# Performance work log

Measured on AMD Instinct MI355X. Metric: run time of the kernel, lower is better.

## Reference

```python
import jax, jax.numpy as jnp
import numpy as np

N, D_IN, D, E, B = 30000, 512, 512, 300000, 4096
N_RES, N_DNN = 2, 2
EPS = 1e-5


def _ln(x, g, b):
    mu = jnp.mean(x, axis=-1, keepdims=True)
    var = jnp.mean((x - mu) ** 2, axis=-1, keepdims=True)
    return (x - mu) * jax.lax.rsqrt(var + EPS) * g + b


def setup_inputs() -> dict:
    key = jax.random.key(0)
    ks = jax.random.split(key, 16)
    s = 1.0 / np.sqrt(D)
    inp = {
        "node_feat": jax.random.normal(ks[0], (N, D_IN), jnp.float32),
        "edge_hop0": jax.random.randint(ks[1], (2, E), 0, N, jnp.int32),
        "edge_hop1": jax.random.randint(ks[2], (2, E), 0, N, jnp.int32),
        "target_idx": jax.random.randint(ks[3], (B,), 0, N, jnp.int32),
        # node transform
        "Wt": jax.random.normal(ks[4], (D_IN, D), jnp.float32) / np.sqrt(D_IN),
        "bt": jnp.zeros((D,), jnp.float32),
        # GATConv (shared across both hops, one relation)
        "Wf": jax.random.normal(ks[5], (D, D), jnp.float32) * s,
        "bf": jnp.zeros((D,), jnp.float32),
        "w_att": jax.random.normal(ks[6], (2 * D,), jnp.float32) * s,
        "b_att": jnp.zeros((), jnp.float32),
        "gat_bias": jnp.zeros((D,), jnp.float32),
        # Res_DNN
        "Wp": jax.random.normal(ks[7], (D, D), jnp.float32) * s,
        "bp": jnp.zeros((D,), jnp.float32),
        "dnn_W": jax.random.normal(ks[8], (N_RES, N_DNN, D, D), jnp.float32) * s,
        "dnn_b": jnp.zeros((N_RES, N_DNN, D), jnp.float32),
        "dnn_g": jnp.ones((N_RES, N_DNN, D), jnp.float32),
        "dnn_beta": jnp.zeros((N_RES, N_DNN, D), jnp.float32),
        "res_g": jnp.ones((N_RES, D), jnp.float32),
        "res_beta": jnp.zeros((N_RES, D), jnp.float32),
        "Wc": jax.random.normal(ks[9], (D, 1), jnp.float32) * s,
        "bc": jnp.zeros((1,), jnp.float32),
    }
    return inp


def _gat(feat, edges, Wf, bf, w_att, b_att, gat_bias):
    # dst and src are the same node set / same features here
    h = feat @ Wf + bf                      # [N, D]
    di, si = edges[0], edges[1]             # [E], [E]
    # att(concat(dst_h, src_h)) == dst_h @ w[:D] + src_h @ w[D:] + b
    sd = h @ w_att[:D]                      # [N]
    ss = h @ w_att[D:]                      # [N]
    e = jnp.tanh(sd[di] + ss[si] + b_att)   # [E]
    # sparse softmax per destination row
    m = jax.ops.segment_max(e, di, num_segments=N)
    a = jnp.exp(e - m[di])
    denom = jax.ops.segment_sum(a, di, num_segments=N)
    alpha = a / denom[di]                   # [E]
    # sparse-mm aggregation
    out = jax.ops.segment_sum(alpha[:, None] * h[si], di, num_segments=N)
    return out + gat_bias


def reference(node_feat, edge_hop0, edge_hop1, target_idx, Wt, bt, Wf, bf,
              w_att, b_att, gat_bias, Wp, bp, dnn_W, dnn_b, dnn_g, dnn_beta,
              res_g, res_beta, Wc, bc):
    # node-type feature transform (dropout is identity at inference)
    feat = node_feat @ Wt + bt              # [N, D]
    # hops processed from last to first: hop1 then hop0
    for edges in (edge_hop1, edge_hop0):
        g = _gat(feat, edges, Wf, bf, w_att, b_att, gat_bias)
        feat = (feat + g) * 0.5             # mean of stacked [orig, gat_out]
    h = feat[target_idx]                    # [B, D]
    # Res_DNN head
    h = h @ Wp + bp
    for r in range(N_RES):
        sc = h
        for i in range(N_DNN):
            h = _ln(jnp.tanh(h @ dnn_W[r, i] + dnn_b[r, i]), dnn_g[r, i], dnn_beta[r, i])
        h = _ln(jnp.tanh(sc + h), res_g[r], res_beta[r])
    logits = h @ Wc + bc                    # [B, 1]
    return jax.nn.sigmoid(logits)
```

## Files before the change

### kernel.cpp

```cpp
#include <hip/hip_runtime.h>

#define D 512
typedef unsigned short ushort_t;
typedef __attribute__((ext_vector_type(8))) short bf16x8;
typedef __attribute__((ext_vector_type(4))) float f32x4;

static __device__ __forceinline__ ushort_t f2bf(float f) {
  unsigned u = __float_as_uint(f);
  u += 0x7fffu + ((u >> 16) & 1u);
  return (ushort_t)(u >> 16);
}
static __device__ __forceinline__ float bf2f(ushort_t h) {
  return __uint_as_float(((unsigned)h) << 16);
}

static __device__ __forceinline__ void gld_lds16(const void* g, void* lds) {
  __builtin_amdgcn_global_load_lds(
      (const __attribute__((address_space(1))) unsigned int*)g,
      (__attribute__((address_space(3))) unsigned int*)lds, 16, 0, 0);
}

__global__ __launch_bounds__(256) void pack_weight7(
    const float* __restrict__ Wt, const float* __restrict__ Wf,
    const float* __restrict__ Wp, const float* __restrict__ Wd,
    ushort_t* __restrict__ out) {
  const int per = D * D;
  int i = blockIdx.x * 256 + threadIdx.x;
  if (i >= per * 7) return;
  const int mat = i / per;
  const int r = i - mat * per;
  const float* W;
  if (mat == 0) W = Wt;
  else if (mat == 1) W = Wf;
  else if (mat == 2) W = Wp;
  else W = Wd + (size_t)(mat - 3) * per;
  const int k = r / D, n = r - k * D;
  const int nt = n >> 4, col = n & 15, kt = k >> 5, kg = (k >> 3) & 3, j = k & 7;
  out[(size_t)mat * per + (((size_t)nt * (D >> 5) + kt) << 9) + ((kg << 4) + col) * 8 + j] =
      f2bf(W[r]);
}

__global__ __launch_bounds__(256) void conv_bf16_pad(
    const float* __restrict__ in, ushort_t* __restrict__ out, int M, int Mp, int K) {
  const size_t i4 = ((size_t)blockIdx.x * 256 + threadIdx.x) * 4;
  if (i4 >= (size_t)Mp * K) return;
  const int row = (int)(i4 / K);
  ushort4 o;
  if (row < M) {
    const float4 v = *reinterpret_cast<const float4*>(&in[i4]);
    o.x = f2bf(v.x); o.y = f2bf(v.y); o.z = f2bf(v.z); o.w = f2bf(v.w);
  } else {
    o.x = o.y = o.z = o.w = 0;
  }
  *reinterpret_cast<ushort4*>(&out[i4]) = o;
}

__global__ __launch_bounds__(256) void init_buffers(
    int* __restrict__ cnt, int* __restrict__ tflag, int* __restrict__ nflag,
    int* __restrict__ counters, int Nn, int N2) {
  const int i = blockIdx.x * 256 + threadIdx.x;
  if (i < N2) cnt[i] = 0;
  if (i < Nn) { tflag[i] = 0; nflag[i] = 0; }
  if (i < 2) counters[i * 64] = 0;
}

__global__ void fill_bucket(const int* __restrict__ e1, const int* __restrict__ e0,
                            const int* __restrict__ tidx, int* __restrict__ tflag,
                            int* __restrict__ cnt, int* __restrict__ bucket,
                            int Nn, int E, int B) {
  const int e = blockIdx.x * blockDim.x + threadIdx.x;
  if (e < B) tflag[tidx[e]] = 1;
  if (e >= E) return;
  const int d1 = e1[e];
  const int p1 = atomicAdd(&cnt[d1], 1);
  if (p1 < 64) bucket[(size_t)d1 * 64 + p1] = e1[E + e];
  const int d0 = e0[e];
  const int p0 = atomicAdd(&cnt[Nn + d0], 1);
  if (p0 < 64) bucket[((size_t)(Nn + d0)) * 64 + p0] = e0[E + e];
}

__global__ void flag_srcs(const int* __restrict__ e0, const int* __restrict__ tflag,
                          int* __restrict__ nflag, int E) {
  const int e = blockIdx.x * blockDim.x + threadIdx.x;
  if (e < E && tflag[e0[e]]) nflag[e0[E + e]] = 1;
}

__global__ void compact2(const int* __restrict__ tflag, const int* __restrict__ nflag,
                         int* __restrict__ tlist, int* __restrict__ nlist,
                         int* __restrict__ counters, int Nn) {
  const int i = blockIdx.x * 256 + threadIdx.x;
  if (i >= Nn) return;
  const int tf = tflag[i];
  if (tf) tlist[atomicAdd(&counters[0], 1)] = i;
  if (tf | nflag[i]) nlist[atomicAdd(&counters[64], 1)] = i;
}

__global__ __launch_bounds__(512) void gemm_mfma(
    const ushort_t* __restrict__ A, const ushort_t* __restrict__ Bp,
    const float* __restrict__ bias, ushort_t* __restrict__ C16,
    const float* __restrict__ watt, float* __restrict__ sd_part,
    float* __restrict__ ss_part, int Mp, int N, int K) {
  __shared__ __align__(16) ushort_t As[2][8 * 512];
  __shared__ __align__(16) ushort_t Bs[2][8 * 512];
  const int nwg = gridDim.x;
  const int q = nwg >> 3, rm = nwg & 7;
  const int xcd = blockIdx.x & 7, kk = blockIdx.x >> 3;
  const int lin = (xcd < rm ? xcd * (q + 1) : rm * (q + 1) + (xcd - rm) * q) + kk;
  const int m0 = (lin >> 2) * 128;
  const int n0 = (lin & 3) * 128;
  const int tid = threadIdx.x;
  const int lane = tid & 63;
  const int wid = tid >> 6;
  const int wm = wid >> 1;
  const int wn = wid & 1;
  const int arow = lane & 15;
  const int akoff = (lane >> 4) * 8;
  const int c15 = lane & 15;
  const int rgrp = lane >> 4;
  const int kt32 = K >> 5;
  f32x4 acc[2][4] = {};

  auto stage = [&](int kt, int b) {
    const int k0 = kt * 32;
    gld_lds16(&A[(size_t)(m0 + wid * 16 + arow) * K + k0 + akoff],
              &As[b][wid * 512]);
    gld_lds16(&Bp[(((size_t)(n0 / 16 + wid) * kt32 + kt) << 9) + lane * 8],
              &Bs[b][wid * 512]);
  };

  stage(0, 0);
  __syncthreads();
  int cur = 0;
  for (int t = 0; t < kt32; ++t) {
    if (t + 1 < kt32) stage(t + 1, cur ^ 1);
    bf16x8 af[2], bfr[4];
#pragma unroll
    for (int mi = 0; mi < 2; ++mi)
      af[mi] = *reinterpret_cast<const bf16x8*>(&As[cur][(wm * 2 + mi) * 512 + lane * 8]);
#pragma unroll
    for (int ni = 0; ni < 4; ++ni)
      bfr[ni] = *reinterpret_cast<const bf16x8*>(&Bs[cur][(wn * 4 + ni) * 512 + lane * 8]);
#pragma unroll
    for (int mi = 0; mi < 2; ++mi)
#pragma unroll
      for (int ni = 0; ni < 4; ++ni)
        acc[mi][ni] = __builtin_amdgcn_mfma_f32_16x16x32_bf16(af[mi], bfr[ni], acc[mi][ni], 0, 0, 0);
    __syncthreads();
    cur ^= 1;
  }
  const int band = (n0 >> 6) + wn;
#pragma unroll
  for (int mi = 0; mi < 2; ++mi) {
    const int row = m0 + wm * 32 + mi * 16 + (rgrp << 2);
#pragma unroll
    for (int r = 0; r < 4; ++r) {
      float psd = 0.f, pss = 0.f;
#pragma unroll
      for (int ni = 0; ni < 4; ++ni) {
        const int col = n0 + wn * 64 + ni * 16 + c15;
        const float v = acc[mi][ni][r] + bias[col];
        C16[(size_t)(row + r) * N + col] = f2bf(v);
        if (watt) {
          psd += v * watt[col];
          pss += v * watt[D + col];
        }
      }
      if (watt) {
#pragma unroll
        for (int off = 8; off > 0; off >>= 1) {
          psd += __shfl_xor(psd, off);
          pss += __shfl_xor(pss, off);
        }
        if (c15 == 0) {
          sd_part[(size_t)band * Mp + row + r] = psd;
          ss_part[(size_t)band * Mp + row + r] = pss;
        }
      }
    }
  }
}

__global__ __launch_bounds__(256) void combine_dots(
    const float* __restrict__ sd_part, const float* __restrict__ ss_part,
    float* __restrict__ sd, float* __restrict__ ss, int Mp, int Nn) {
  const int i = blockIdx.x * 256 + threadIdx.x;
  if (i >= Nn) return;
  float a = 0.f, b = 0.f;
#pragma unroll
  for (int bnd = 0; bnd < 8; ++bnd) {
    a += sd_part[(size_t)bnd * Mp + i];
    b += ss_part[(size_t)bnd * Mp + i];
  }
  sd[i] = a;
  ss[i] = b;
}

__global__ __launch_bounds__(256) void gat_aggregate_w(
    ushort_t* __restrict__ featb, const ushort_t* __restrict__ hb,
    const float* __restrict__ sd, const float* __restrict__ ss,
    const int* __restrict__ di, const int* __restrict__ si,
    const float* __restrict__ b_att_p, const float* __restrict__ gat_bias,
    const int* __restrict__ cnt, const int* __restrict__ bucket,
    const int* __restrict__ dstlist, const int* __restrict__ dcount,
    int Nn, int E) {
  const int gidx = blockIdx.x * 4 + (threadIdx.x >> 6);
  const int lane = threadIdx.x & 63;
  if (gidx >= *dcount) return;
  const int dst = dstlist[gidx];
  const int deg = cnt[dst];
  const float sdd = sd[dst];
  const float ba = b_att_p[0];
  const size_t o = (size_t)dst * D + lane * 8;
  bf16x8 fv = *reinterpret_cast<const bf16x8*>(&featb[o]);
  float acc[8] = {};
  if (deg <= 64) {
    const bool valid = lane < deg;
    const int slane = valid ? bucket[(size_t)dst * 64 + lane] : 0;
    const float e = valid ? tanhf(sdd + ss[slane] + ba) : -1e30f;
    float m = e;
#pragma unroll
    for (int off = 32; off > 0; off >>= 1) m = fmaxf(m, __shfl_xor(m, off));
    const float a = valid ? expf(e - m) : 0.f;
    float s = a;
#pragma unroll
    for (int off = 32; off > 0; off >>= 1) s += __shfl_xor(s, off);
    const float w = a * ((s > 0.f) ? 1.f / s : 0.f);
    int k = 0;
    for (; k + 3 < deg; k += 4) {
      const float w0 = __shfl(w, k), w1 = __shfl(w, k + 1);
      const float w2 = __shfl(w, k + 2), w3 = __shfl(w, k + 3);
      const int s0 = __shfl(slane, k), s1 = __shfl(slane, k + 1);
      const int s2 = __shfl(slane, k + 2), s3 = __shfl(slane, k + 3);
      const bf16x8 h0 = *reinterpret_cast<const bf16x8*>(&hb[(size_t)s0 * D + lane * 8]);
      const bf16x8 h1 = *reinterpret_cast<const bf16x8*>(&hb[(size_t)s1 * D + lane * 8]);
      const bf16x8 h2 = *reinterpret_cast<const bf16x8*>(&hb[(size_t)s2 * D + lane * 8]);
      const bf16x8 h3 = *reinterpret_cast<const bf16x8*>(&hb[(size_t)s3 * D + lane * 8]);
#pragma unroll
      for (int qq = 0; qq < 8; ++qq) {
        const float t0 = w0 * bf2f((ushort_t)h0[qq]) + w1 * bf2f((ushort_t)h1[qq]);
        const float t1 = w2 * bf2f((ushort_t)h2[qq]) + w3 * bf2f((ushort_t)h3[qq]);
        acc[qq] += t0 + t1;
      }
    }
    for (; k < deg; ++k) {
      const float wk = __shfl(w, k);
      const int sk = __shfl(slane, k);
      const bf16x8 h0 = *reinterpret_cast<const bf16x8*>(&hb[(size_t)sk * D + lane * 8]);
#pragma unroll
      for (int qq = 0; qq < 8; ++qq) acc[qq] += wk * bf2f((ushort_t)h0[qq]);
    }
  } else {
    float m = -1e30f;
    for (int e = lane; e < E; e += 64)
      if (di[e] == dst) m = fmaxf(m, tanhf(sdd + ss[si[e]] + ba));
#pragma unroll
    for (int off = 32; off > 0; off >>= 1) m = fmaxf(m, __shfl_xor(m, off));
    float s = 0.f;
    for (int e = lane; e < E; e += 64)
      if (di[e] == dst) s += expf(tanhf(sdd + ss[si[e]] + ba) - m);
#pragma unroll
    for (int off = 32; off > 0; off >>= 1) s += __shfl_xor(s, off);
    const float inv = (s > 0.f) ? 1.f / s : 0.f;
    for (int base = 0; base < E; base += 64) {
      const int e = base + lane;
      const bool hit = (e < E) && (di[e] == dst);
      unsigned long long mask = __ballot(hit);
      const int sidx = hit ? si[e] : 0;
      const float aval = hit ? expf(tanhf(sdd + ss[sidx] + ba) - m) * inv : 0.f;
      while (mask) {
        const int l = __ffsll((long long)mask) - 1;
        mask &= mask - 1;
        const float wv = __shfl(aval, l);
        const int sk = __shfl(sidx, l);
        const bf16x8 hv = *reinterpret_cast<const bf16x8*>(&hb[(size_t)sk * D + lane * 8]);
#pragma unroll
        for (int qq = 0; qq < 8; ++qq) acc[qq] += wv * bf2f((ushort_t)hv[qq]);
      }
    }
  }
#pragma unroll
  for (int q = 0; q < 8; ++q) {
    const float f = (bf2f((ushort_t)fv[q]) + acc[q] + gat_bias[lane * 8 + q]) * 0.5f;
    fv[q] = (short)f2bf(f);
  }
  *reinterpret_cast<bf16x8*>(&featb[o]) = fv;
}

__global__ __launch_bounds__(512, 4) void head_fused(
    const ushort_t* __restrict__ featb, const int* __restrict__ tidx,
    const ushort_t* __restrict__ pWp, const float* __restrict__ bp,
    const ushort_t* __restrict__ pDW, const float* __restrict__ dnn_b,
    const float* __restrict__ dnn_g, const float* __restrict__ dnn_be,
    const float* __restrict__ res_g, const float* __restrict__ res_be,
    const float* __restrict__ Wc, const float* __restrict__ bc,
    float* __restrict__ out) {
  __shared__ __align__(16) ushort_t A_lds[16 * 512];
  __shared__ float lsum[8][8], lsq[8][8], meanv[8], rsv[8];
  const int tid = threadIdx.x;
  const int lane = tid & 63;
  const int wave = tid >> 6;
  const int nt0 = wave * 4;
  const int c15 = lane & 15;
  const int rgrp = lane >> 4;

  {
    const int row = tid >> 6, col8 = tid & 63;
    const int g = tidx[blockIdx.x * 8 + row];
    const bf16x8 v = *reinterpret_cast<const bf16x8*>(&featb[(size_t)g * D + col8 * 8]);
    *reinterpret_cast<bf16x8*>(&A_lds[row * 512 + (col8 ^ (row & 7)) * 8]) = v;
    const int rz = row + 8;
    *reinterpret_cast<bf16x8*>(&A_lds[rz * 512 + (col8 ^ (rz & 7)) * 8]) = bf16x8{};
  }
  __syncthreads();

  auto do_gemm = [&](const ushort_t* __restrict__ W, f32x4* a) {
#pragma unroll
    for (int ni = 0; ni < 4; ++ni) a[ni] = f32x4{0.f, 0.f, 0.f, 0.f};
#pragma unroll
    for (int kt = 0; kt < 16; ++kt) {
      const int col8 = kt * 4 + rgrp;
      const bf16x8 af = *reinterpret_cast<const bf16x8*>(
          &A_lds[c15 * 512 + (col8 ^ (c15 & 7)) * 8]);
#pragma unroll
      for (int ni = 0; ni < 4; ++ni) {
        const bf16x8 w = *reinterpret_cast<const bf16x8*>(
            &W[(((size_t)(nt0 + ni) * 16 + kt) << 9) + lane * 8]);
        a[ni] = __builtin_amdgcn_mfma_f32_16x16x32_bf16(af, w, a[ni], 0, 0, 0);
      }
    }
  };

  auto block_ln = [&](f32x4* v, const float* __restrict__ g,
                      const float* __restrict__ be) {
    float psum[4], psq[4];
#pragma unroll
    for (int r = 0; r < 4; ++r) { psum[r] = 0.f; psq[r] = 0.f; }
#pragma unroll
    for (int ni = 0; ni < 4; ++ni)
#pragma unroll
      for (int r = 0; r < 4; ++r) {
        psum[r] += v[ni][r];
        psq[r] += v[ni][r] * v[ni][r];
      }
#pragma unroll
    for (int off = 8; off > 0; off >>= 1)
#pragma unroll
      for (int r = 0; r < 4; ++r) {
        psum[r] += __shfl_xor(psum[r], off);
        psq[r] += __shfl_xor(psq[r], off);
      }
    if (c15 == 0 && rgrp < 2) {
#pragma unroll
      for (int r = 0; r < 4; ++r) {
        lsum[wave][rgrp * 4 + r] = psum[r];
        lsq[wave][rgrp * 4 + r] = psq[r];
      }
    }
    __syncthreads();
    if (tid < 8) {
      float s = 0.f, qq = 0.f;
#pragma unroll
      for (int w = 0; w < 8; ++w) { s += lsum[w][tid]; qq += lsq[w][tid]; }
      const float mean = s * (1.f / 512.f);
      const float var = qq * (1.f / 512.f) - mean * mean;
      meanv[tid] = mean;
      rsv[tid] = rsqrtf(var + 1e-5f);
    }
    __syncthreads();
#pragma unroll
    for (int ni = 0; ni < 4; ++ni) {
      const int col = (nt0 + ni) * 16 + c15;
      const float gg = g[col], bb = be[col];
#pragma unroll
      for (int r = 0; r < 4; ++r) {
        const int row = (rgrp * 4 + r) & 7;
        v[ni][r] = (v[ni][r] - meanv[row]) * rsv[row] * gg + bb;
      }
    }
  };

  auto store_A = [&](const f32x4* v) {
    if (rgrp >= 2) return;
#pragma unroll
    for (int ni = 0; ni < 4; ++ni) {
      const int col = (nt0 + ni) * 16 + c15;
#pragma unroll
      for (int r = 0; r < 4; ++r) {
        const int row = rgrp * 4 + r;
        A_lds[row * 512 + (((col >> 3) ^ (row & 7)) << 3) + (col & 7)] = f2bf(v[ni][r]);
      }
    }
  };

  f32x4 sc[4], acc[4], ln[4];

  do_gemm(pWp, acc);
#pragma unroll
  for (int ni = 0; ni < 4; ++ni) {
    const float bv = bp[(nt0 + ni) * 16 + c15];
#pragma unroll
    for (int r = 0; r < 4; ++r) sc[ni][r] = acc[ni][r] + bv;
  }
  __syncthreads();
  store_A(sc);
  __syncthreads();

  for (int rb = 0; rb < 2; ++rb) {
    {
      const int st = rb * 2;
      do_gemm(pDW + (size_t)st * D * D, acc);
#pragma unroll
      for (int ni = 0; ni < 4; ++ni) {
        const float bv = dnn_b[st * D + (nt0 + ni) * 16 + c15];
#pragma unroll
        for (int r = 0; r < 4; ++r) acc[ni][r] = tanhf(acc[ni][r] + bv);
      }
      block_ln(acc, dnn_g + st * D, dnn_be + st * D);
      store_A(acc);
      __syncthreads();
    }
    {
      const int st = rb * 2 + 1;
      do_gemm(pDW + (size_t)st * D * D, ln);
#pragma unroll
      for (int ni = 0; ni < 4; ++ni) {
        const float bv = dnn_b[st * D + (nt0 + ni) * 16 + c15];
#pragma unroll
        for (int r = 0; r < 4; ++r) ln[ni][r] = tanhf(ln[ni][r] + bv);
      }
      block_ln(ln, dnn_g + st * D, dnn_be + st * D);
    }
#pragma unroll
    for (int ni = 0; ni < 4; ++ni)
#pragma unroll
      for (int r = 0; r < 4; ++r) acc[ni][r] = tanhf(sc[ni][r] + ln[ni][r]);
    block_ln(acc, res_g + rb * D, res_be + rb * D);
#pragma unroll
    for (int ni = 0; ni < 4; ++ni) sc[ni] = acc[ni];
    if (rb == 0) {
      store_A(sc);
      __syncthreads();
    }
  }

  float pr[4];
#pragma unroll
  for (int r = 0; r < 4; ++r) pr[r] = 0.f;
#pragma unroll
  for (int ni = 0; ni < 4; ++ni) {
    const float wv = Wc[(nt0 + ni) * 16 + c15];
#pragma unroll
    for (int r = 0; r < 4; ++r) pr[r] += sc[ni][r] * wv;
  }
#pragma unroll
  for (int off = 8; off > 0; off >>= 1)
#pragma unroll
    for (int r = 0; r < 4; ++r) pr[r] += __shfl_xor(pr[r], off);
  __syncthreads();
  if (c15 == 0 && rgrp < 2) {
#pragma unroll
    for (int r = 0; r < 4; ++r) lsum[wave][rgrp * 4 + r] = pr[r];
  }
  __syncthreads();
  if (tid < 8) {
    float s = 0.f;
#pragma unroll
    for (int w = 0; w < 8; ++w) s += lsum[w][tid];
    out[blockIdx.x * 8 + tid] = 1.f / (1.f + expf(-(s + bc[0])));
  }
}

extern "C" void kernel_launch(void* const* d_in, const int* in_sizes, int n_in,
                              void* d_out, int out_size, void* d_ws, size_t ws_size,
                              hipStream_t stream) {
  (void)n_in; (void)out_size; (void)ws_size;
  const float* node_feat = (const float*)d_in[0];
  const int* edge0 = (const int*)d_in[1];
  const int* edge1 = (const int*)d_in[2];
  const int* tidx = (const int*)d_in[3];
  const float* Wt = (const float*)d_in[4];
  const float* bt = (const float*)d_in[5];
  const float* Wf = (const float*)d_in[6];
  const float* bfp = (const float*)d_in[7];
  const float* w_att = (const float*)d_in[8];
  const float* b_att = (const float*)d_in[9];
  const float* gat_bias = (const float*)d_in[10];
  const float* Wp = (const float*)d_in[11];
  const float* bp = (const float*)d_in[12];
  const float* dnn_W = (const float*)d_in[13];
  const float* dnn_b = (const float*)d_in[14];
  const float* dnn_g = (const float*)d_in[15];
  const float* dnn_be = (const float*)d_in[16];
  const float* res_g = (const float*)d_in[17];
  const float* res_be = (const float*)d_in[18];
  const float* Wc = (const float*)d_in[19];
  const float* bc = (const float*)d_in[20];
  float* out = (float*)d_out;

  const int Nn = in_sizes[0] / D;
  const int E = in_sizes[1] / 2;
  const int B = in_sizes[3];
  const int K_IN = in_sizes[4] / D;
  const int Mp = (Nn + 127) / 128 * 128;
  const int N2 = 2 * Nn;

  char* p = (char*)d_ws;
  auto alloc = [&](size_t bytes) -> char* {
    char* r = p;
    p += (bytes + 255) & ~(size_t)255;
    return r;
  };
  ushort_t* featb = (ushort_t*)alloc((size_t)Mp * D * 2);
  ushort_t* hb = (ushort_t*)alloc((size_t)Mp * D * 2);
  float* sd = (float*)alloc((size_t)Nn * 4);
  float* ss = (float*)alloc((size_t)Nn * 4);
  float* sd_part = (float*)alloc((size_t)8 * Mp * 4);
  float* ss_part = (float*)alloc((size_t)8 * Mp * 4);
  int* cnt = (int*)alloc((size_t)N2 * 4);
  int* bucket = (int*)alloc((size_t)N2 * 64 * 4);
  int* tflag = (int*)alloc((size_t)Nn * 4);
  int* nflag = (int*)alloc((size_t)Nn * 4);
  int* tlist = (int*)alloc((size_t)B * 4);
  int* nlist = (int*)alloc((size_t)Nn * 4);
  int* counters = (int*)alloc(512);
  ushort_t* pAll = (ushort_t*)alloc((size_t)7 * D * D * 2);
  ushort_t* pWt = pAll;
  ushort_t* pWf = pAll + (size_t)D * D;
  ushort_t* pWp = pAll + (size_t)2 * D * D;
  ushort_t* pDWall = pAll + (size_t)3 * D * D;

  dim3 blk(256);

  pack_weight7<<<(7 * D * D + 255) / 256, blk, 0, stream>>>(Wt, Wf, Wp, dnn_W, pAll);
  conv_bf16_pad<<<((size_t)Mp * K_IN / 4 + 255) / 256, blk, 0, stream>>>(
      node_feat, hb , Nn, Mp, K_IN);

  init_buffers<<<(N2 + 255) / 256, blk, 0, stream>>>(cnt, tflag, nflag, counters, Nn, N2);
  fill_bucket<<<(E + 255) / 256, blk, 0, stream>>>(edge1, edge0, tidx, tflag,
                                                   cnt, bucket, Nn, E, B);
  flag_srcs<<<(E + 255) / 256, blk, 0, stream>>>(edge0, tflag, nflag, E);
  compact2<<<(Nn + 255) / 256, blk, 0, stream>>>(tflag, nflag, tlist, nlist,
                                                 counters, Nn);

  gemm_mfma<<<dim3(4 * (Mp / 128)), dim3(512), 0, stream>>>(
      hb, pWt, bt, featb, nullptr, nullptr, nullptr, Mp, D, K_IN);

  const int* hops[2] = {edge1, edge0};
  for (int hp = 0; hp < 2; ++hp) {
    gemm_mfma<<<dim3(4 * (Mp / 128)), dim3(512), 0, stream>>>(
        featb, pWf, bfp, hb, w_att, sd_part, ss_part, Mp, D, D);
    combine_dots<<<(Nn + 255) / 256, blk, 0, stream>>>(sd_part, ss_part, sd, ss, Mp, Nn);
    if (hp == 0) {
      gat_aggregate_w<<<(Nn + 3) / 4, blk, 0, stream>>>(
          featb, hb, sd, ss, hops[hp], hops[hp] + E, b_att, gat_bias,
          cnt + hp * Nn, bucket + (size_t)hp * Nn * 64, nlist, &counters[64], Nn, E);
    } else {
      gat_aggregate_w<<<(B + 3) / 4, blk, 0, stream>>>(
          featb, hb, sd, ss, hops[hp], hops[hp] + E, b_att, gat_bias,
          cnt + hp * Nn, bucket + (size_t)hp * Nn * 64, tlist, &counters[0], Nn, E);
    }
  }

  head_fused<<<B / 8, dim3(512), 0, stream>>>(
      featb, tidx, pWp, bp, pDWall, dnn_b, dnn_g, dnn_be, res_g, res_be,
      Wc, bc, out);
}
```

Baseline: 339.2 us.

## Process 32 rows per head block with 16 waves to raise weight reuse

The fused MLP head now handles 32 target rows per block with 1024 threads instead of 8 real rows padded to 16 with 512 threads. Each wave computes a 2x2 grid of MFMA tiles, so every weight fragment loaded from global memory is reused across two 16-row M tiles and the zero-padded half of the MFMA tile is no longer wasted. Weight traffic per output row drops about fourfold. In exchange there are 128 blocks instead of 512, which lowers grid-level parallelism, and the larger block has to synchronise more waves at each LayerNorm barrier.

```diff
diff --git a/kernel.cpp b/kernel.cpp
--- a/kernel.cpp
+++ b/kernel.cpp
@@ -286,7 +286,7 @@
   *reinterpret_cast<bf16x8*>(&featb[o]) = fv;
 }
 
-__global__ __launch_bounds__(512, 4) void head_fused(
+__global__ __launch_bounds__(1024, 4) void head_fused(
     const ushort_t* __restrict__ featb, const int* __restrict__ tidx,
     const ushort_t* __restrict__ pWp, const float* __restrict__ bp,
     const ushort_t* __restrict__ pDW, const float* __restrict__ dnn_b,
@@ -294,73 +294,79 @@
     const float* __restrict__ res_g, const float* __restrict__ res_be,
     const float* __restrict__ Wc, const float* __restrict__ bc,
     float* __restrict__ out) {
-  __shared__ __align__(16) ushort_t A_lds[16 * 512];
-  __shared__ float lsum[8][8], lsq[8][8], meanv[8], rsv[8];
+  __shared__ __align__(16) ushort_t A_lds[32 * 512];
+  __shared__ float lsum[16][32], lsq[16][32], meanv[32], rsv[32];
   const int tid = threadIdx.x;
   const int lane = tid & 63;
   const int wave = tid >> 6;
-  const int nt0 = wave * 4;
+  const int nt0 = wave * 2;
   const int c15 = lane & 15;
   const int rgrp = lane >> 4;
 
   {
-    const int row = tid >> 6, col8 = tid & 63;
-    const int g = tidx[blockIdx.x * 8 + row];
-    const bf16x8 v = *reinterpret_cast<const bf16x8*>(&featb[(size_t)g * D + col8 * 8]);
-    *reinterpret_cast<bf16x8*>(&A_lds[row * 512 + (col8 ^ (row & 7)) * 8]) = v;
-    const int rz = row + 8;
-    *reinterpret_cast<bf16x8*>(&A_lds[rz * 512 + (col8 ^ (rz & 7)) * 8]) = bf16x8{};
+    const int row = tid >> 5;
+    const int col8 = (tid & 31) * 2;
+    const int g = tidx[blockIdx.x * 32 + row];
+    const bf16x8 v0 = *reinterpret_cast<const bf16x8*>(&featb[(size_t)g * D + col8 * 8]);
+    const bf16x8 v1 = *reinterpret_cast<const bf16x8*>(&featb[(size_t)g * D + (col8 + 1) * 8]);
+    *reinterpret_cast<bf16x8*>(&A_lds[row * 512 + (col8 ^ (row & 7)) * 8]) = v0;
+    *reinterpret_cast<bf16x8*>(&A_lds[row * 512 + ((col8 + 1) ^ (row & 7)) * 8]) = v1;
   }
   __syncthreads();
 
-  auto do_gemm = [&](const ushort_t* __restrict__ W, f32x4* a) {
-#pragma unroll
-    for (int ni = 0; ni < 4; ++ni) a[ni] = f32x4{0.f, 0.f, 0.f, 0.f};
+  auto do_gemm = [&](const ushort_t* __restrict__ W, f32x4 a[2][2]) {
+#pragma unroll
+    for (int mi = 0; mi < 2; ++mi)
+#pragma unroll
+      for (int ni = 0; ni < 2; ++ni) a[mi][ni] = f32x4{0.f, 0.f, 0.f, 0.f};
 #pragma unroll
     for (int kt = 0; kt < 16; ++kt) {
       const int col8 = kt * 4 + rgrp;
-      const bf16x8 af = *reinterpret_cast<const bf16x8*>(
+      const bf16x8 af0 = *reinterpret_cast<const bf16x8*>(
           &A_lds[c15 * 512 + (col8 ^ (c15 & 7)) * 8]);
-#pragma unroll
-      for (int ni = 0; ni < 4; ++ni) {
-        const bf16x8 w = *reinterpret_cast<const bf16x8*>(
-            &W[(((size_t)(nt0 + ni) * 16 + kt) << 9) + lane * 8]);
-        a[ni] = __builtin_amdgcn_mfma_f32_16x16x32_bf16(af, w, a[ni], 0, 0, 0);
-      }
+      const bf16x8 af1 = *reinterpret_cast<const bf16x8*>(
+          &A_lds[(16 + c15) * 512 + (col8 ^ (c15 & 7)) * 8]);
+      const bf16x8 w0 = *reinterpret_cast<const bf16x8*>(
+          &W[(((size_t)nt0 * 16 + kt) << 9) + lane * 8]);
+      const bf16x8 w1 = *reinterpret_cast<const bf16x8*>(
+          &W[(((size_t)(nt0 + 1) * 16 + kt) << 9) + lane * 8]);
+      a[0][0] = __builtin_amdgcn_mfma_f32_16x16x32_bf16(af0, w0, a[0][0], 0, 0, 0);
+      a[0][1] = __builtin_amdgcn_mfma_f32_16x16x32_bf16(af0, w1, a[0][1], 0, 0, 0);
+      a[1][0] = __builtin_amdgcn_mfma_f32_16x16x32_bf16(af1, w0, a[1][0], 0, 0, 0);
+      a[1][1] = __builtin_amdgcn_mfma_f32_16x16x32_bf16(af1, w1, a[1][1], 0, 0, 0);
     }
   };
 
-  auto block_ln = [&](f32x4* v, const float* __restrict__ g,
+  auto block_ln = [&](f32x4 v[2][2], const float* __restrict__ g,
                       const float* __restrict__ be) {
-    float psum[4], psq[4];
-#pragma unroll
-    for (int r = 0; r < 4; ++r) { psum[r] = 0.f; psq[r] = 0.f; }
-#pragma unroll
-    for (int ni = 0; ni < 4; ++ni)
+#pragma unroll
+    for (int mi = 0; mi < 2; ++mi) {
+      float psum[4], psq[4];
 #pragma unroll
       for (int r = 0; r < 4; ++r) {
-        psum[r] += v[ni][r];
-        psq[r] += v[ni][r] * v[ni][r];
-      }
-#pragma unroll
-    for (int off = 8; off > 0; off >>= 1)
-#pragma unroll
-      for (int r = 0; r < 4; ++r) {
-        psum[r] += __shfl_xor(psum[r], off);
-        psq[r] += __shfl_xor(psq[r], off);
-      }
-    if (c15 == 0 && rgrp < 2) {
-#pragma unroll
-      for (int r = 0; r < 4; ++r) {
-        lsum[wave][rgrp * 4 + r] = psum[r];
-        lsq[wave][rgrp * 4 + r] = psq[r];
+        psum[r] = v[mi][0][r] + v[mi][1][r];
+        psq[r] = v[mi][0][r] * v[mi][0][r] + v[mi][1][r] * v[mi][1][r];
+      }
+#pragma unroll
+      for (int off = 8; off > 0; off >>= 1)
+#pragma unroll
+        for (int r = 0; r < 4; ++r) {
+          psum[r] += __shfl_xor(psum[r], off);
+          psq[r] += __shfl_xor(psq[r], off);
+        }
+      if (c15 == 0) {
+#pragma unroll
+        for (int r = 0; r < 4; ++r) {
+          lsum[wave][mi * 16 + rgrp * 4 + r] = psum[r];
+          lsq[wave][mi * 16 + rgrp * 4 + r] = psq[r];
+        }
       }
     }
     __syncthreads();
-    if (tid < 8) {
+    if (tid < 32) {
       float s = 0.f, qq = 0.f;
 #pragma unroll
-      for (int w = 0; w < 8; ++w) { s += lsum[w][tid]; qq += lsq[w][tid]; }
+      for (int w = 0; w < 16; ++w) { s += lsum[w][tid]; qq += lsq[w][tid]; }
       const float mean = s * (1.f / 512.f);
       const float var = qq * (1.f / 512.f) - mean * mean;
       meanv[tid] = mean;
@@ -368,38 +374,44 @@
     }
     __syncthreads();
 #pragma unroll
-    for (int ni = 0; ni < 4; ++ni) {
+    for (int ni = 0; ni < 2; ++ni) {
       const int col = (nt0 + ni) * 16 + c15;
       const float gg = g[col], bb = be[col];
 #pragma unroll
-      for (int r = 0; r < 4; ++r) {
-        const int row = (rgrp * 4 + r) & 7;
-        v[ni][r] = (v[ni][r] - meanv[row]) * rsv[row] * gg + bb;
-      }
+      for (int mi = 0; mi < 2; ++mi)
+#pragma unroll
+        for (int r = 0; r < 4; ++r) {
+          const int row = mi * 16 + rgrp * 4 + r;
+          v[mi][ni][r] = (v[mi][ni][r] - meanv[row]) * rsv[row] * gg + bb;
+        }
     }
   };
 
-  auto store_A = [&](const f32x4* v) {
-    if (rgrp >= 2) return;
-#pragma unroll
-    for (int ni = 0; ni < 4; ++ni) {
+  auto store_A = [&](const f32x4 v[2][2]) {
+#pragma unroll
+    for (int ni = 0; ni < 2; ++ni) {
       const int col = (nt0 + ni) * 16 + c15;
 #pragma unroll
-      for (int r = 0; r < 4; ++r) {
-        const int row = rgrp * 4 + r;
-        A_lds[row * 512 + (((col >> 3) ^ (row & 7)) << 3) + (col & 7)] = f2bf(v[ni][r]);
-      }
+      for (int mi = 0; mi < 2; ++mi)
+#pragma unroll
+        for (int r = 0; r < 4; ++r) {
+          const int row = mi * 16 + rgrp * 4 + r;
+          A_lds[row * 512 + (((col >> 3) ^ (row & 7)) << 3) + (col & 7)] =
+              f2bf(v[mi][ni][r]);
+        }
     }
   };
 
-  f32x4 sc[4], acc[4], ln[4];
+  f32x4 sc[2][2], acc[2][2], ln[2][2];
 
   do_gemm(pWp, acc);
 #pragma unroll
-  for (int ni = 0; ni < 4; ++ni) {
+  for (int ni = 0; ni < 2; ++ni) {
     const float bv = bp[(nt0 + ni) * 16 + c15];
 #pragma unroll
-    for (int r = 0; r < 4; ++r) sc[ni][r] = acc[ni][r] + bv;
+    for (int mi = 0; mi < 2; ++mi)
+#pragma unroll
+      for (int r = 0; r < 4; ++r) sc[mi][ni][r] = acc[mi][ni][r] + bv;
   }
   __syncthreads();
   store_A(sc);
@@ -410,10 +422,12 @@
       const int st = rb * 2;
       do_gemm(pDW + (size_t)st * D * D, acc);
 #pragma unroll
-      for (int ni = 0; ni < 4; ++ni) {
+      for (int ni = 0; ni < 2; ++ni) {
         const float bv = dnn_b[st * D + (nt0 + ni) * 16 + c15];
 #pragma unroll
-        for (int r = 0; r < 4; ++r) acc[ni][r] = tanhf(acc[ni][r] + bv);
+        for (int mi = 0; mi < 2; ++mi)
+#pragma unroll
+          for (int r = 0; r < 4; ++r) acc[mi][ni][r] = tanhf(acc[mi][ni][r] + bv);
       }
       block_ln(acc, dnn_g + st * D, dnn_be + st * D);
       store_A(acc);
@@ -423,50 +437,60 @@
       const int st = rb * 2 + 1;
       do_gemm(pDW + (size_t)st * D * D, ln);
 #pragma unroll
-      for (int ni = 0; ni < 4; ++ni) {
+      for (int ni = 0; ni < 2; ++ni) {
         const float bv = dnn_b[st * D + (nt0 + ni) * 16 + c15];
 #pragma unroll
-        for (int r = 0; r < 4; ++r) ln[ni][r] = tanhf(ln[ni][r] + bv);
+        for (int mi = 0; mi < 2; ++mi)
+#pragma unroll
+          for (int r = 0; r < 4; ++r) ln[mi][ni][r] = tanhf(ln[mi][ni][r] + bv);
       }
       block_ln(ln, dnn_g + st * D, dnn_be + st * D);
     }
 #pragma unroll
-    for (int ni = 0; ni < 4; ++ni)
-#pragma unroll
-      for (int r = 0; r < 4; ++r) acc[ni][r] = tanhf(sc[ni][r] + ln[ni][r]);
+    for (int mi = 0; mi < 2; ++mi)
+#pragma unroll
+      for (int ni = 0; ni < 2; ++ni)
+#pragma unroll
+        for (int r = 0; r < 4; ++r)
+          acc[mi][ni][r] = tanhf(sc[mi][ni][r] + ln[mi][ni][r]);
     block_ln(acc, res_g + rb * D, res_be + rb * D);
 #pragma unroll
-    for (int ni = 0; ni < 4; ++ni) sc[ni] = acc[ni];
+    for (int mi = 0; mi < 2; ++mi)
+#pragma unroll
+      for (int ni = 0; ni < 2; ++ni) sc[mi][ni] = acc[mi][ni];
     if (rb == 0) {
       store_A(sc);
       __syncthreads();
     }
   }
 
-  float pr[4];
-#pragma unroll
-  for (int r = 0; r < 4; ++r) pr[r] = 0.f;
-#pragma unroll
-  for (int ni = 0; ni < 4; ++ni) {
-    const float wv = Wc[(nt0 + ni) * 16 + c15];
-#pragma unroll
-    for (int r = 0; r < 4; ++r) pr[r] += sc[ni][r] * wv;
-  }
-#pragma unroll
-  for (int off = 8; off > 0; off >>= 1)
-#pragma unroll
-    for (int r = 0; r < 4; ++r) pr[r] += __shfl_xor(pr[r], off);
+#pragma unroll
+  for (int mi = 0; mi < 2; ++mi) {
+    float pr[4];
+#pragma unroll
+    for (int r = 0; r < 4; ++r) pr[r] = 0.f;
+#pragma unroll
+    for (int ni = 0; ni < 2; ++ni) {
+      const float wv = Wc[(nt0 + ni) * 16 + c15];
+#pragma unroll
+      for (int r = 0; r < 4; ++r) pr[r] += sc[mi][ni][r] * wv;
+    }
+#pragma unroll
+    for (int off = 8; off > 0; off >>= 1)
+#pragma unroll
+      for (int r = 0; r < 4; ++r) pr[r] += __shfl_xor(pr[r], off);
+    if (mi == 0) __syncthreads();
+    if (c15 == 0) {
+#pragma unroll
+      for (int r = 0; r < 4; ++r) lsum[wave][mi * 16 + rgrp * 4 + r] = pr[r];
+    }
+  }
   __syncthreads();
-  if (c15 == 0 && rgrp < 2) {
-#pragma unroll
-    for (int r = 0; r < 4; ++r) lsum[wave][rgrp * 4 + r] = pr[r];
-  }
-  __syncthreads();
-  if (tid < 8) {
+  if (tid < 32) {
     float s = 0.f;
 #pragma unroll
-    for (int w = 0; w < 8; ++w) s += lsum[w][tid];
-    out[blockIdx.x * 8 + tid] = 1.f / (1.f + expf(-(s + bc[0])));
+    for (int w = 0; w < 16; ++w) s += lsum[w][tid];
+    out[blockIdx.x * 32 + tid] = 1.f / (1.f + expf(-(s + bc[0])));
   }
 }
 
@@ -561,7 +585,7 @@
     }
   }
 
-  head_fused<<<B / 8, dim3(512), 0, stream>>>(
+  head_fused<<<B / 32, dim3(1024), 0, stream>>>(
       featb, tidx, pWp, bp, pDWall, dnn_b, dnn_g, dnn_be, res_g, res_be,
       Wc, bc, out);
 }
```

After: 311.5 us. 1.09x faster.
